# Kernel optimization log

Hardware: AMD Instinct MI355X
Metric: run time of the kernel (lower is better)

The kernel has to match this reference:

```python
import math
import jax, jax.numpy as jnp
import numpy as np

B, S, HID, H, NREL = 4, 512, 1024, 16, 64
D = HID // H  # per-head size = 64, must equal relation embedding dim


def setup_inputs() -> dict:
    key = jax.random.key(0)
    ks = jax.random.split(key, 12)
    w = lambda k, shape: jax.random.normal(k, shape, jnp.float32) * 0.02
    return {
        "q_in": jax.random.normal(ks[0], (B, S, HID), jnp.float32),
        "k_in": jax.random.normal(ks[1], (B, S, HID), jnp.float32),
        "v_in": jax.random.normal(ks[2], (B, S, HID), jnp.float32),
        "mask": jax.random.randint(ks[3], (B, 1, S, S), 0, NREL),
        "Wq": w(ks[4], (HID, HID)), "bq": jnp.zeros((HID,), jnp.float32),
        "Wk": w(ks[5], (HID, HID)), "bk": jnp.zeros((HID,), jnp.float32),
        "Wv": w(ks[6], (HID, HID)), "bv": jnp.zeros((HID,), jnp.float32),
        "Wo": w(ks[7], (HID, HID)), "bo": jnp.zeros((HID,), jnp.float32),
        "rel_k_table": w(ks[8], (NREL, D)),
        "rel_v_table": w(ks[9], (NREL, D)),
    }


def reference(q_in, k_in, v_in, mask, Wq, bq, Wk, bk, Wv, bv, Wo, bo,
              rel_k_table, rel_v_table):
    def proj(x, W, b):  # [B,S,HID] -> [B,H,S,D]
        return (x @ W.T + b).reshape(B, S, H, D).transpose(0, 2, 1, 3)

    q = proj(q_in, Wq, bq)
    k = proj(k_in, Wk, bk)
    v = proj(v_in, Wv, bv)

    ids = mask[:, 0]                      # [B,S,S] relation ids
    rel_k = rel_k_table[ids]              # [B,S,S,D]
    rel_v = rel_v_table[ids]              # [B,S,S,D]

    scores = jnp.einsum('bhqd,bhkd->bhqk', q, k)
    scores = scores + jnp.einsum('bhqd,bqkd->bhqk', q, rel_k) / 4.0
    scores = scores / math.sqrt(float(D))

    bias = (1.0 - (mask > 0).astype(scores.dtype)) * -10000.0  # [B,1,S,S]
    probs = jax.nn.softmax(scores + bias, axis=-1)             # [B,H,S,S]

    out = jnp.einsum('bhqk,bhkd->bhqd', probs, v)
    out = out + 0.25 * jnp.einsum('bhqk,bqkd->bhqd', probs, rel_v)
    out = out.transpose(0, 2, 1, 3).reshape(B, S, HID)
    return out @ Wo.T + bo
```

## Files before the change

kernel.cpp:

```cpp
#include <hip/hip_runtime.h>


typedef __attribute__((ext_vector_type(8))) short bf16x8 __attribute__((may_alias));
typedef __attribute__((ext_vector_type(4))) float f32x4;

__device__ __forceinline__ short f2bf(float x) {
    unsigned u = __float_as_uint(x);
    u += 0x7fff + ((u >> 16) & 1);
    return (short)(u >> 16);
}

__device__ __forceinline__ void async16(void* lds, const void* g) {
    __builtin_amdgcn_global_load_lds(
        (const __attribute__((address_space(1))) void*)g,
        (__attribute__((address_space(3))) void*)lds, 16, 0, 0);
}

__global__ __launch_bounds__(256)
void cast_all(const float* __restrict__ x0, const float* __restrict__ x1, const float* __restrict__ x2,
              const float* __restrict__ w0, const float* __restrict__ w1,
              const float* __restrict__ w2, const float* __restrict__ w3,
              const float* __restrict__ rk, const float* __restrict__ rv,
              const int* __restrict__ mask,
              short* __restrict__ y0, short* __restrict__ y1, short* __restrict__ y2,
              short* __restrict__ u0, short* __restrict__ u1,
              short* __restrict__ u2, short* __restrict__ u3,
              short* __restrict__ rkb, short* __restrict__ rvT,
              unsigned char* __restrict__ mu8)
{
    size_t i = (size_t)blockIdx.x * 256 + threadIdx.x;
    if (i < 2621440u) {
        const float* src; short* dst; size_t off;
        if (i < 3u*524288u) {
            int s = (int)(i / 524288u); off = i % 524288u;
            src = s == 0 ? x0 : (s == 1 ? x1 : x2);
            dst = s == 0 ? y0 : (s == 1 ? y1 : y2);
        } else {
            size_t j = i - 3u*524288u;
            int s = (int)(j / 262144u); off = j % 262144u;
            src = s == 0 ? w0 : (s == 1 ? w1 : (s == 2 ? w2 : w3));
            dst = s == 0 ? u0 : (s == 1 ? u1 : (s == 2 ? u2 : u3));
        }
        float4 f = ((const float4*)src)[off];
        short4 o; o.x = f2bf(f.x); o.y = f2bf(f.y); o.z = f2bf(f.z); o.w = f2bf(f.w);
        ((short4*)dst)[off] = o;
    } else if (i < 2621440u + 1024u) {
        size_t off = i - 2621440u;
        float4 f = ((const float4*)rk)[off];
        short4 o; o.x = f2bf(f.x); o.y = f2bf(f.y); o.z = f2bf(f.z); o.w = f2bf(f.w);
        ((short4*)rkb)[off] = o;
    } else if (i < 2622464u + 1024u) {
        int m = (int)(i - 2622464u);
        int d = m >> 4, r0 = (m & 15) * 4;
        short4 o;
        o.x = f2bf(rv[(size_t)(r0 + 0) * 64 + d]);
        o.y = f2bf(rv[(size_t)(r0 + 1) * 64 + d]);
        o.z = f2bf(rv[(size_t)(r0 + 2) * 64 + d]);
        o.w = f2bf(rv[(size_t)(r0 + 3) * 64 + d]);
        *(short4*)&rvT[d * 64 + r0] = o;
    } else if (i < 2623488u + 262144u) {
        size_t m = i - 2623488u;
        int4 v = ((const int4*)mask)[m];
        uchar4 o;
        o.x = (unsigned char)v.x; o.y = (unsigned char)v.y;
        o.z = (unsigned char)v.z; o.w = (unsigned char)v.w;
        ((uchar4*)mu8)[m] = o;
    }
}

__global__ __launch_bounds__(256)
void gemm12864(const short* __restrict__ A0, const short* __restrict__ A1, const short* __restrict__ A2,
               const short* __restrict__ B0, const short* __restrict__ B1, const short* __restrict__ B2,
               const float* __restrict__ c0, const float* __restrict__ c1, const float* __restrict__ c2,
               void* __restrict__ O0, void* __restrict__ O1, void* __restrict__ O2,
               int mode)
{
    __shared__ short ldsw[2 * 12288];

    const int z = blockIdx.z;
    const short* A    = z == 0 ? A0 : (z == 1 ? A1 : A2);
    const short* Bm   = z == 0 ? B0 : (z == 1 ? B1 : B2);
    const float* bias = z == 0 ? c0 : (z == 1 ? c1 : c2);
    void*        O    = z == 0 ? O0 : (z == 1 ? O1 : O2);

    const int t = threadIdx.x;
    const int lane = t & 63, w = t >> 6;
    const int wr = w >> 1, wc = w & 1;
    const int quad = lane >> 4, cl = lane & 15;
    const int rowBase = blockIdx.y * 128;
    const int colBase = blockIdx.x * 64;
    const int gl = ((lane & 7) - (lane >> 3)) & 7;

    f32x4 acc[4][2];
#pragma unroll
    for (int i = 0; i < 4; ++i)
#pragma unroll
        for (int j = 0; j < 2; ++j) acc[i][j] = (f32x4){0.f, 0.f, 0.f, 0.f};

    const int rstage = w * 8 + (lane >> 3);
    const short* Ag = A  + (size_t)(rowBase + rstage) * 1024 + gl * 8;
    const short* Bg = Bm + (size_t)(colBase + rstage) * 1024 + gl * 8;

    {
        short* Als = ldsw;
        short* Bls = ldsw + 8192;
#pragma unroll
        for (int i = 0; i < 4; ++i)
            async16(&Als[(i * 32 + w * 8) * 64], Ag + (size_t)i * 32 * 1024);
#pragma unroll
        for (int i = 0; i < 2; ++i)
            async16(&Bls[(i * 32 + w * 8) * 64], Bg + (size_t)i * 32 * 1024);
    }

    for (int it = 0; it < 16; ++it) {
        const int cur = it & 1;
        __syncthreads();
        if (it < 15) {
            short* Als = ldsw + (cur ^ 1) * 12288;
            short* Bls = Als + 8192;
            const int k0 = (it + 1) * 64;
#pragma unroll
            for (int i = 0; i < 4; ++i)
                async16(&Als[(i * 32 + w * 8) * 64], Ag + (size_t)i * 32 * 1024 + k0);
#pragma unroll
            for (int i = 0; i < 2; ++i)
                async16(&Bls[(i * 32 + w * 8) * 64], Bg + (size_t)i * 32 * 1024 + k0);
        }
        const short* Als = ldsw + cur * 12288;
        const short* Bls = Als + 8192;
#pragma unroll
        for (int kk = 0; kk < 2; ++kk) {
            bf16x8 a[4], b[2];
#pragma unroll
            for (int mi = 0; mi < 4; ++mi) {
                int r = wr * 64 + mi * 16 + cl;
                int s = (kk * 4 + quad + r) & 7;
                a[mi] = *(const bf16x8*)&Als[r * 64 + s * 8];
            }
#pragma unroll
            for (int ni = 0; ni < 2; ++ni) {
                int r = wc * 32 + ni * 16 + cl;
                int s = (kk * 4 + quad + r) & 7;
                b[ni] = *(const bf16x8*)&Bls[r * 64 + s * 8];
            }
#pragma unroll
            for (int mi = 0; mi < 4; ++mi)
#pragma unroll
                for (int ni = 0; ni < 2; ++ni)
                    acc[mi][ni] = __builtin_amdgcn_mfma_f32_16x16x32_bf16(
                        a[mi], b[ni], acc[mi][ni], 0, 0, 0);
        }
    }

    if (mode == 0) {
#pragma unroll
        for (int mi = 0; mi < 4; ++mi)
#pragma unroll
            for (int ni = 0; ni < 2; ++ni) {
                int col = colBase + wc * 32 + ni * 16 + cl;
                float bv = bias[col];
#pragma unroll
                for (int reg = 0; reg < 4; ++reg) {
                    int row = rowBase + wr * 64 + mi * 16 + quad * 4 + reg;
                    ((float*)O)[(size_t)row * 1024 + col] = acc[mi][ni][reg] + bv;
                }
            }
        return;
    }

    __syncthreads();
    short* Tls = ldsw;
    if (z == 2) {
#pragma unroll
        for (int mi = 0; mi < 4; ++mi)
#pragma unroll
            for (int ni = 0; ni < 2; ++ni) {
                int d = wc * 32 + ni * 16 + cl;
                float bv = bias[colBase + d];
                short4 pk;
                pk.x = f2bf(acc[mi][ni][0] + bv);
                pk.y = f2bf(acc[mi][ni][1] + bv);
                pk.z = f2bf(acc[mi][ni][2] + bv);
                pk.w = f2bf(acc[mi][ni][3] + bv);
                int sl = wr * 64 + mi * 16 + quad * 4;
                *(short4*)&Tls[d * 136 + sl] = pk;
            }
        __syncthreads();
        int d = t >> 2, s0 = (t & 3) * 32;
        int bb = rowBase >> 9, sBase = rowBase & 511, hh = colBase >> 6;
        short* dst = (short*)O + (((size_t)(bb * 16 + hh) * 64 + d) << 9) + sBase + s0;
#pragma unroll
        for (int j = 0; j < 4; ++j)
            *(bf16x8*)(dst + j * 8) = *(const bf16x8*)&Tls[d * 136 + s0 + j * 8];
    } else {
#pragma unroll
        for (int mi = 0; mi < 4; ++mi)
#pragma unroll
            for (int ni = 0; ni < 2; ++ni) {
                int d = wc * 32 + ni * 16 + cl;
                float bv = bias[colBase + d];
#pragma unroll
                for (int reg = 0; reg < 4; ++reg) {
                    int sl = wr * 64 + mi * 16 + quad * 4 + reg;
                    Tls[sl * 72 + d] = f2bf(acc[mi][ni][reg] + bv);
                }
            }
        __syncthreads();
        int sl = t >> 1, half = t & 1;
        int bb = rowBase >> 9, sBase = rowBase & 511, hh = colBase >> 6;
        short* dst = (short*)O + (((size_t)(bb * 16 + hh) * 512 + sBase + sl) << 6) + half * 32;
#pragma unroll
        for (int j = 0; j < 4; ++j)
            *(bf16x8*)(dst + j * 8) = *(const bf16x8*)&Tls[sl * 72 + half * 32 + j * 8];
    }
}

#define AT_BINS 4352
#define AT_PST  8704
#define AT_SLICE 11264

__global__ __launch_bounds__(256)
void attn_kernel(const short* __restrict__ qg, const short* __restrict__ kg,
                 const short* __restrict__ vtg, const unsigned char* __restrict__ mu8,
                 const short* __restrict__ relkb, const short* __restrict__ relvT,
                 short* __restrict__ attn_b)
{
    __shared__ __align__(16) char pool[4 * AT_SLICE];
    const int t = threadIdx.x;
    const int lane = t & 63, w = t >> 6;
    char* mypool = pool + w * AT_SLICE;
    float* qwr    = (float*)mypool;
    float* bins   = (float*)(mypool + AT_BINS);
    short* Pst    = (short*)(mypool + AT_PST);
    short* binsBf = Pst;

    const int quad = lane >> 4, cl = lane & 15;
    const int bid = blockIdx.x;
    const int bh = bid & 63, qq = bid >> 6;
    const int b = bh >> 4, h = bh & 15, q0 = qq * 64 + w * 16;

    const short* qbase = qg  + ((size_t)bh * 512 + q0) * 64;
    const short* kbase = kg  + (size_t)bh * 512 * 64;
    const short* vbase = vtg + (size_t)bh * 64 * 512;
    const unsigned char* mb = mu8 + (size_t)b * 512 * 512 + (size_t)q0 * 512;

    for (int i = lane; i < 16 * 68; i += 64) bins[i] = 0.f;

    bf16x8 qa0 = *(const bf16x8*)(qbase + cl * 64 + quad * 8);
    bf16x8 qa1 = *(const bf16x8*)(qbase + cl * 64 + 32 + quad * 8);

#pragma unroll
    for (int rt = 0; rt < 4; ++rt) {
        const short* kp = relkb + (size_t)(rt * 16 + cl) * 64 + quad * 8;
        bf16x8 rb0 = *(const bf16x8*)kp;
        bf16x8 rb1 = *(const bf16x8*)(kp + 32);
        f32x4 qr = (f32x4){0.f, 0.f, 0.f, 0.f};
        qr = __builtin_amdgcn_mfma_f32_16x16x32_bf16(qa0, rb0, qr, 0, 0, 0);
        qr = __builtin_amdgcn_mfma_f32_16x16x32_bf16(qa1, rb1, qr, 0, 0, 0);
#pragma unroll
        for (int reg = 0; reg < 4; ++reg)
            qwr[(quad * 4 + reg) * 68 + rt * 16 + cl] = qr[reg];
    }

    f32x4 oacc[4];
#pragma unroll
    for (int dt = 0; dt < 4; ++dt) oacc[dt] = (f32x4){0.f, 0.f, 0.f, 0.f};
    float lpart[4] = {0.f, 0.f, 0.f, 0.f};

    for (int c = 0; c < 8; ++c) {
        const int k0 = c * 64;
        int ids[4][4];
#pragma unroll
        for (int nt = 0; nt < 4; ++nt)
#pragma unroll
            for (int reg = 0; reg < 4; ++reg)
                ids[nt][reg] = mb[(size_t)(quad * 4 + reg) * 512 + k0 + nt * 16 + cl];

        bf16x8 vb[8];
#pragma unroll
        for (int dt = 0; dt < 4; ++dt) {
            const short* vp = vbase + (size_t)(dt * 16 + cl) * 512 + k0 + quad * 8;
            vb[dt * 2]     = *(const bf16x8*)vp;
            vb[dt * 2 + 1] = *(const bf16x8*)(vp + 32);
        }

#pragma unroll
        for (int nt = 0; nt < 4; ++nt) {
            const int kidx = k0 + nt * 16 + cl;
            const short* kp = kbase + (size_t)kidx * 64 + quad * 8;
            bf16x8 kb0 = *(const bf16x8*)kp;
            bf16x8 kb1 = *(const bf16x8*)(kp + 32);
            f32x4 s = (f32x4){0.f, 0.f, 0.f, 0.f};
            __builtin_amdgcn_s_setprio(1);
            s = __builtin_amdgcn_mfma_f32_16x16x32_bf16(qa0, kb0, s, 0, 0, 0);
            s = __builtin_amdgcn_mfma_f32_16x16x32_bf16(qa1, kb1, s, 0, 0, 0);
            __builtin_amdgcn_s_setprio(0);
#pragma unroll
            for (int reg = 0; reg < 4; ++reg) {
                int q = quad * 4 + reg;
                int id = ids[nt][reg];
                float sc = (s[reg] + 0.25f * qwr[q * 68 + id]) * 0.125f;
                float p = (id == 0) ? 0.f : __expf(sc);
                lpart[reg] += p;
                atomicAdd(&bins[q * 68 + id], p);
                Pst[q * 72 + nt * 16 + cl] = f2bf(p);
            }
        }
        bf16x8 pa0 = *(const bf16x8*)&Pst[cl * 72 + quad * 8];
        bf16x8 pa1 = *(const bf16x8*)&Pst[cl * 72 + 32 + quad * 8];
        __builtin_amdgcn_s_setprio(1);
#pragma unroll
        for (int dt = 0; dt < 4; ++dt) {
            oacc[dt] = __builtin_amdgcn_mfma_f32_16x16x32_bf16(pa0, vb[dt * 2],     oacc[dt], 0, 0, 0);
            oacc[dt] = __builtin_amdgcn_mfma_f32_16x16x32_bf16(pa1, vb[dt * 2 + 1], oacc[dt], 0, 0, 0);
        }
        __builtin_amdgcn_s_setprio(0);
    }

    float invq[4];
#pragma unroll
    for (int reg = 0; reg < 4; ++reg) {
        float l = lpart[reg];
#pragma unroll
        for (int m = 8; m >= 1; m >>= 1) l += __shfl_xor(l, m);
        invq[reg] = 1.0f / l;
    }

    {
        int q = lane >> 2, r0 = (lane & 3) * 16;
#pragma unroll
        for (int j = 0; j < 4; ++j) {
            float4 f = *(const float4*)&bins[q * 68 + r0 + j * 4];
            short4 o;
            o.x = f2bf(f.x); o.y = f2bf(f.y); o.z = f2bf(f.z); o.w = f2bf(f.w);
            *(short4*)&binsBf[q * 72 + r0 + j * 4] = o;
        }
    }

    bf16x8 ba0 = *(const bf16x8*)&binsBf[cl * 72 + quad * 8];
    bf16x8 ba1 = *(const bf16x8*)&binsBf[cl * 72 + 32 + quad * 8];
#pragma unroll
    for (int dt = 0; dt < 4; ++dt) {
        const short* rp = relvT + (size_t)(dt * 16 + cl) * 64 + quad * 8;
        bf16x8 rv0 = *(const bf16x8*)rp;
        bf16x8 rv1 = *(const bf16x8*)(rp + 32);
        f32x4 racc = (f32x4){0.f, 0.f, 0.f, 0.f};
        racc = __builtin_amdgcn_mfma_f32_16x16x32_bf16(ba0, rv0, racc, 0, 0, 0);
        racc = __builtin_amdgcn_mfma_f32_16x16x32_bf16(ba1, rv1, racc, 0, 0, 0);
#pragma unroll
        for (int reg = 0; reg < 4; ++reg) {
            int q = quad * 4 + reg;
            float val = (oacc[dt][reg] + 0.25f * racc[reg]) * invq[reg];
            attn_b[(size_t)(b * 512 + q0 + q) * 1024 + h * 64 + dt * 16 + cl] = f2bf(val);
        }
    }
}

extern "C" void kernel_launch(void* const* d_in, const int* in_sizes, int n_in,
                              void* d_out, int out_size, void* d_ws, size_t ws_size,
                              hipStream_t stream)
{
    const float* q_in = (const float*)d_in[0];
    const float* k_in = (const float*)d_in[1];
    const float* v_in = (const float*)d_in[2];
    const int*   mask = (const int*)d_in[3];
    const float* Wq   = (const float*)d_in[4];
    const float* bq   = (const float*)d_in[5];
    const float* Wk   = (const float*)d_in[6];
    const float* bk   = (const float*)d_in[7];
    const float* Wv   = (const float*)d_in[8];
    const float* bv   = (const float*)d_in[9];
    const float* Wo   = (const float*)d_in[10];
    const float* bo   = (const float*)d_in[11];
    const float* relk = (const float*)d_in[12];
    const float* relv = (const float*)d_in[13];

    char* ws = (char*)d_ws;
    short* qb     = (short*)(ws);
    short* kb     = (short*)(ws + (4u  << 20));
    short* vt     = (short*)(ws + (8u  << 20));
    short* attn_b = (short*)(ws + (12u << 20));
    short* Xq     = (short*)(ws + (16u << 20));
    short* Xk     = (short*)(ws + (20u << 20));
    short* Xv     = (short*)(ws + (24u << 20));
    short* Wqb    = (short*)(ws + (28u << 20));
    short* Wkb    = (short*)(ws + (30u << 20));
    short* Wvb    = (short*)(ws + (32u << 20));
    short* Wob    = (short*)(ws + (34u << 20));
    short* relkb  = (short*)(ws + (36u << 20));
    short* relvT  = (short*)(ws + (36u << 20) + 8192);
    unsigned char* masku8 = (unsigned char*)(ws + (36u << 20) + 16384);

    cast_all<<<11272, 256, 0, stream>>>(q_in, k_in, v_in, Wq, Wk, Wv, Wo, relk, relv, mask,
                                        Xq, Xk, Xv, Wqb, Wkb, Wvb, Wob, relkb, relvT, masku8);

    gemm12864<<<dim3(16, 16, 3), 256, 0, stream>>>(
        Xq, Xk, Xv, Wqb, Wkb, Wvb, bq, bk, bv, qb, kb, vt, 1);

    attn_kernel<<<dim3(512), 256, 0, stream>>>(qb, kb, vt, masku8, relkb, relvT, attn_b);

    gemm12864<<<dim3(16, 16, 1), 256, 0, stream>>>(
        attn_b, attn_b, attn_b, Wob, Wob, Wob, bo, bo, bo,
        (void*)d_out, (void*)d_out, (void*)d_out, 0);
}
```

Baseline: 236.4 us.

## Stage K and V tiles in LDS with double-buffered async loads

The attention kernel now loads each 64-key K chunk and V^T chunk into shared LDS buffers with async global-to-LDS copies, split across the four waves. It uses XOR-swizzled layouts and double buffering, so the next chunk is prefetched while the current one is computed. This removes the redundant per-wave global reads of K and V, which were previously repeated four times per block. In exchange it adds a block-wide barrier per chunk and more LDS per block, which may lower occupancy.

```diff
diff --git a/kernel.cpp b/kernel.cpp
--- a/kernel.cpp
+++ b/kernel.cpp
@@ -215,9 +215,9 @@
     }
 }
 
-#define AT_BINS 4352
-#define AT_PST  8704
-#define AT_SLICE 11264
+#define AT_KV    16384
+#define AT_WSLC  11264
+#define AT_TOT   (2 * AT_KV + 4 * AT_WSLC)
 
 __global__ __launch_bounds__(256)
 void attn_kernel(const short* __restrict__ qg, const short* __restrict__ kg,
@@ -225,16 +225,16 @@
                  const short* __restrict__ relkb, const short* __restrict__ relvT,
                  short* __restrict__ attn_b)
 {
-    __shared__ __align__(16) char pool[4 * AT_SLICE];
+    __shared__ __align__(16) char pool[AT_TOT];
     const int t = threadIdx.x;
     const int lane = t & 63, w = t >> 6;
-    char* mypool = pool + w * AT_SLICE;
+    const int quad = lane >> 4, cl = lane & 15;
+    char* mypool = pool + 2 * AT_KV + w * AT_WSLC;
     float* qwr    = (float*)mypool;
-    float* bins   = (float*)(mypool + AT_BINS);
-    short* Pst    = (short*)(mypool + AT_PST);
+    float* bins   = (float*)(mypool + 4352);
+    short* Pst    = (short*)(mypool + 8704);
     short* binsBf = Pst;
 
-    const int quad = lane >> 4, cl = lane & 15;
     const int bid = blockIdx.x;
     const int bh = bid & 63, qq = bid >> 6;
     const int b = bh >> 4, h = bh & 15, q0 = qq * 64 + w * 16;
@@ -244,7 +244,18 @@
     const short* vbase = vtg + (size_t)bh * 64 * 512;
     const unsigned char* mb = mu8 + (size_t)b * 512 * 512 + (size_t)q0 * 512;
 
+    const int rA = w * 16 + (lane >> 3);
+    const int rB = rA + 8;
+    const int mmS = lane & 7;
+    const int cA = (mmS ^ (rA & 7)) << 3;
+    const int cB = (mmS ^ (rB & 7)) << 3;
+
     for (int i = lane; i < 16 * 68; i += 64) bins[i] = 0.f;
+
+    async16(pool + w * 2048,               kbase + (size_t)rA * 64 + cA);
+    async16(pool + w * 2048 + 1024,        kbase + (size_t)rB * 64 + cB);
+    async16(pool + 8192 + w * 2048,        vbase + (size_t)rA * 512 + cA);
+    async16(pool + 8192 + w * 2048 + 1024, vbase + (size_t)rB * 512 + cB);
 
     bf16x8 qa0 = *(const bf16x8*)(qbase + cl * 64 + quad * 8);
     bf16x8 qa1 = *(const bf16x8*)(qbase + cl * 64 + 32 + quad * 8);
@@ -268,7 +279,19 @@
     float lpart[4] = {0.f, 0.f, 0.f, 0.f};
 
     for (int c = 0; c < 8; ++c) {
+        const int cur = c & 1;
         const int k0 = c * 64;
+        __syncthreads();
+
+        if (c < 7) {
+            const int k1 = k0 + 64;
+            char* nb = pool + (cur ^ 1) * AT_KV;
+            async16(nb + w * 2048,               kbase + (size_t)(k1 + rA) * 64 + cA);
+            async16(nb + w * 2048 + 1024,        kbase + (size_t)(k1 + rB) * 64 + cB);
+            async16(nb + 8192 + w * 2048,        vbase + (size_t)rA * 512 + k1 + cA);
+            async16(nb + 8192 + w * 2048 + 1024, vbase + (size_t)rB * 512 + k1 + cB);
+        }
+
         int ids[4][4];
 #pragma unroll
         for (int nt = 0; nt < 4; ++nt)
@@ -276,20 +299,14 @@
             for (int reg = 0; reg < 4; ++reg)
                 ids[nt][reg] = mb[(size_t)(quad * 4 + reg) * 512 + k0 + nt * 16 + cl];
 
-        bf16x8 vb[8];
-#pragma unroll
-        for (int dt = 0; dt < 4; ++dt) {
-            const short* vp = vbase + (size_t)(dt * 16 + cl) * 512 + k0 + quad * 8;
-            vb[dt * 2]     = *(const bf16x8*)vp;
-            vb[dt * 2 + 1] = *(const bf16x8*)(vp + 32);
-        }
+        const char* Kt = pool + cur * AT_KV;
+        const char* Vt = Kt + 8192;
 
 #pragma unroll
         for (int nt = 0; nt < 4; ++nt) {
-            const int kidx = k0 + nt * 16 + cl;
-            const short* kp = kbase + (size_t)kidx * 64 + quad * 8;
-            bf16x8 kb0 = *(const bf16x8*)kp;
-            bf16x8 kb1 = *(const bf16x8*)(kp + 32);
+            const int rk = nt * 16 + cl;
+            bf16x8 kb0 = *(const bf16x8*)(Kt + rk * 128 + ((quad ^ (rk & 7)) << 4));
+            bf16x8 kb1 = *(const bf16x8*)(Kt + rk * 128 + (((quad + 4) ^ (rk & 7)) << 4));
             f32x4 s = (f32x4){0.f, 0.f, 0.f, 0.f};
             __builtin_amdgcn_s_setprio(1);
             s = __builtin_amdgcn_mfma_f32_16x16x32_bf16(qa0, kb0, s, 0, 0, 0);
@@ -311,8 +328,11 @@
         __builtin_amdgcn_s_setprio(1);
 #pragma unroll
         for (int dt = 0; dt < 4; ++dt) {
-            oacc[dt] = __builtin_amdgcn_mfma_f32_16x16x32_bf16(pa0, vb[dt * 2],     oacc[dt], 0, 0, 0);
-            oacc[dt] = __builtin_amdgcn_mfma_f32_16x16x32_bf16(pa1, vb[dt * 2 + 1], oacc[dt], 0, 0, 0);
+            const int rv = dt * 16 + cl;
+            bf16x8 vb0 = *(const bf16x8*)(Vt + rv * 128 + ((quad ^ (rv & 7)) << 4));
+            bf16x8 vb1 = *(const bf16x8*)(Vt + rv * 128 + (((quad + 4) ^ (rv & 7)) << 4));
+            oacc[dt] = __builtin_amdgcn_mfma_f32_16x16x32_bf16(pa0, vb0, oacc[dt], 0, 0, 0);
+            oacc[dt] = __builtin_amdgcn_mfma_f32_16x16x32_bf16(pa1, vb1, oacc[dt], 0, 0, 0);
         }
         __builtin_amdgcn_s_setprio(0);
     }
```

Measured after the change: 237.2 us. Within noise of the previous version (+0.3%).

## Split attention key range across two waves per query tile and grid-stride cast kernel

Applied to the files above, without the earlier changes.

The attention kernel now gives each block a single 16-query tile handled by two waves, each covering half of the 512 keys. A shared-memory reduction then combines the partial outputs, row sums and relation bins before the rel_v MFMA and the store. The grid grows from 512 to 2048 blocks of 128 threads, which gives more parallelism and shorter per-wave loops on the GPU's many CUs. The cost is two block barriers and duplicated q·rel_k work per wave. The cast kernel also switches to a grid-stride loop over 2048 blocks.

```diff
diff --git a/kernel.cpp b/kernel.cpp
--- a/kernel.cpp
+++ b/kernel.cpp
@@ -16,6 +16,7 @@
         (__attribute__((address_space(3))) void*)lds, 16, 0, 0);
 }
 
+#define CAST_TOTAL 2885632u
 __global__ __launch_bounds__(256)
 void cast_all(const float* __restrict__ x0, const float* __restrict__ x1, const float* __restrict__ x2,
               const float* __restrict__ w0, const float* __restrict__ w1,
@@ -28,43 +29,45 @@
               short* __restrict__ rkb, short* __restrict__ rvT,
               unsigned char* __restrict__ mu8)
 {
-    size_t i = (size_t)blockIdx.x * 256 + threadIdx.x;
-    if (i < 2621440u) {
-        const float* src; short* dst; size_t off;
-        if (i < 3u*524288u) {
-            int s = (int)(i / 524288u); off = i % 524288u;
-            src = s == 0 ? x0 : (s == 1 ? x1 : x2);
-            dst = s == 0 ? y0 : (s == 1 ? y1 : y2);
+    const size_t stride = (size_t)gridDim.x * 256;
+    for (size_t i = (size_t)blockIdx.x * 256 + threadIdx.x; i < CAST_TOTAL; i += stride) {
+        if (i < 2621440u) {
+            const float* src; short* dst; size_t off;
+            if (i < 3u*524288u) {
+                int s = (int)(i / 524288u); off = i % 524288u;
+                src = s == 0 ? x0 : (s == 1 ? x1 : x2);
+                dst = s == 0 ? y0 : (s == 1 ? y1 : y2);
+            } else {
+                size_t j = i - 3u*524288u;
+                int s = (int)(j / 262144u); off = j % 262144u;
+                src = s == 0 ? w0 : (s == 1 ? w1 : (s == 2 ? w2 : w3));
+                dst = s == 0 ? u0 : (s == 1 ? u1 : (s == 2 ? u2 : u3));
+            }
+            float4 f = ((const float4*)src)[off];
+            short4 o; o.x = f2bf(f.x); o.y = f2bf(f.y); o.z = f2bf(f.z); o.w = f2bf(f.w);
+            ((short4*)dst)[off] = o;
+        } else if (i < 2621440u + 1024u) {
+            size_t off = i - 2621440u;
+            float4 f = ((const float4*)rk)[off];
+            short4 o; o.x = f2bf(f.x); o.y = f2bf(f.y); o.z = f2bf(f.z); o.w = f2bf(f.w);
+            ((short4*)rkb)[off] = o;
+        } else if (i < 2622464u + 1024u) {
+            int m = (int)(i - 2622464u);
+            int d = m >> 4, r0 = (m & 15) * 4;
+            short4 o;
+            o.x = f2bf(rv[(size_t)(r0 + 0) * 64 + d]);
+            o.y = f2bf(rv[(size_t)(r0 + 1) * 64 + d]);
+            o.z = f2bf(rv[(size_t)(r0 + 2) * 64 + d]);
+            o.w = f2bf(rv[(size_t)(r0 + 3) * 64 + d]);
+            *(short4*)&rvT[d * 64 + r0] = o;
         } else {
-            size_t j = i - 3u*524288u;
-            int s = (int)(j / 262144u); off = j % 262144u;
-            src = s == 0 ? w0 : (s == 1 ? w1 : (s == 2 ? w2 : w3));
-            dst = s == 0 ? u0 : (s == 1 ? u1 : (s == 2 ? u2 : u3));
-        }
-        float4 f = ((const float4*)src)[off];
-        short4 o; o.x = f2bf(f.x); o.y = f2bf(f.y); o.z = f2bf(f.z); o.w = f2bf(f.w);
-        ((short4*)dst)[off] = o;
-    } else if (i < 2621440u + 1024u) {
-        size_t off = i - 2621440u;
-        float4 f = ((const float4*)rk)[off];
-        short4 o; o.x = f2bf(f.x); o.y = f2bf(f.y); o.z = f2bf(f.z); o.w = f2bf(f.w);
-        ((short4*)rkb)[off] = o;
-    } else if (i < 2622464u + 1024u) {
-        int m = (int)(i - 2622464u);
-        int d = m >> 4, r0 = (m & 15) * 4;
-        short4 o;
-        o.x = f2bf(rv[(size_t)(r0 + 0) * 64 + d]);
-        o.y = f2bf(rv[(size_t)(r0 + 1) * 64 + d]);
-        o.z = f2bf(rv[(size_t)(r0 + 2) * 64 + d]);
-        o.w = f2bf(rv[(size_t)(r0 + 3) * 64 + d]);
-        *(short4*)&rvT[d * 64 + r0] = o;
-    } else if (i < 2623488u + 262144u) {
-        size_t m = i - 2623488u;
-        int4 v = ((const int4*)mask)[m];
-        uchar4 o;
-        o.x = (unsigned char)v.x; o.y = (unsigned char)v.y;
-        o.z = (unsigned char)v.z; o.w = (unsigned char)v.w;
-        ((uchar4*)mu8)[m] = o;
+            size_t m = i - 2623488u;
+            int4 v = ((const int4*)mask)[m];
+            uchar4 o;
+            o.x = (unsigned char)v.x; o.y = (unsigned char)v.y;
+            o.z = (unsigned char)v.z; o.w = (unsigned char)v.w;
+            ((uchar4*)mu8)[m] = o;
+        }
     }
 }
 
@@ -215,29 +218,32 @@
     }
 }
 
-#define AT_BINS 4352
-#define AT_PST  8704
-#define AT_SLICE 11264
-
-__global__ __launch_bounds__(256)
+#define AT_QWR   0
+#define AT_BINS  4352
+#define AT_PST   13056
+#define AT_TOT   17664
+
+__global__ __launch_bounds__(128, 4)
 void attn_kernel(const short* __restrict__ qg, const short* __restrict__ kg,
                  const short* __restrict__ vtg, const unsigned char* __restrict__ mu8,
                  const short* __restrict__ relkb, const short* __restrict__ relvT,
                  short* __restrict__ attn_b)
 {
-    __shared__ __align__(16) char pool[4 * AT_SLICE];
+    __shared__ __align__(16) char pool[AT_TOT];
     const int t = threadIdx.x;
     const int lane = t & 63, w = t >> 6;
-    char* mypool = pool + w * AT_SLICE;
-    float* qwr    = (float*)mypool;
-    float* bins   = (float*)(mypool + AT_BINS);
-    short* Pst    = (short*)(mypool + AT_PST);
-    short* binsBf = Pst;
-
     const int quad = lane >> 4, cl = lane & 15;
+
+    float* qwr    = (float*)(pool + AT_QWR);
+    float* bins   = (float*)(pool + AT_BINS + w * 4352);
+    short* Pst    = (short*)(pool + AT_PST  + w * 2304);
+    float* qwrF   = (float*)(pool + AT_QWR);
+    float* lsum1  = (float*)(pool + AT_PST + 2304);
+    short* binsBf = (short*)(pool + AT_PST);
+
     const int bid = blockIdx.x;
-    const int bh = bid & 63, qq = bid >> 6;
-    const int b = bh >> 4, h = bh & 15, q0 = qq * 64 + w * 16;
+    const int bh = bid & 63, qt = bid >> 6;
+    const int b = bh >> 4, h = bh & 15, q0 = qt * 16;
 
     const short* qbase = qg  + ((size_t)bh * 512 + q0) * 64;
     const short* kbase = kg  + (size_t)bh * 512 * 64;
@@ -267,8 +273,8 @@
     for (int dt = 0; dt < 4; ++dt) oacc[dt] = (f32x4){0.f, 0.f, 0.f, 0.f};
     float lpart[4] = {0.f, 0.f, 0.f, 0.f};
 
-    for (int c = 0; c < 8; ++c) {
-        const int k0 = c * 64;
+    for (int c = 0; c < 4; ++c) {
+        const int k0 = w * 256 + c * 64;
         int ids[4][4];
 #pragma unroll
         for (int nt = 0; nt < 4; ++nt)
@@ -317,41 +323,74 @@
         __builtin_amdgcn_s_setprio(0);
     }
 
-    float invq[4];
+    float lred[4];
 #pragma unroll
     for (int reg = 0; reg < 4; ++reg) {
         float l = lpart[reg];
 #pragma unroll
         for (int m = 8; m >= 1; m >>= 1) l += __shfl_xor(l, m);
-        invq[reg] = 1.0f / l;
-    }
-
-    {
-        int q = lane >> 2, r0 = (lane & 3) * 16;
-#pragma unroll
-        for (int j = 0; j < 4; ++j) {
-            float4 f = *(const float4*)&bins[q * 68 + r0 + j * 4];
-            short4 o;
-            o.x = f2bf(f.x); o.y = f2bf(f.y); o.z = f2bf(f.z); o.w = f2bf(f.w);
-            *(short4*)&binsBf[q * 72 + r0 + j * 4] = o;
-        }
-    }
-
-    bf16x8 ba0 = *(const bf16x8*)&binsBf[cl * 72 + quad * 8];
-    bf16x8 ba1 = *(const bf16x8*)&binsBf[cl * 72 + 32 + quad * 8];
-#pragma unroll
-    for (int dt = 0; dt < 4; ++dt) {
-        const short* rp = relvT + (size_t)(dt * 16 + cl) * 64 + quad * 8;
-        bf16x8 rv0 = *(const bf16x8*)rp;
-        bf16x8 rv1 = *(const bf16x8*)(rp + 32);
-        f32x4 racc = (f32x4){0.f, 0.f, 0.f, 0.f};
-        racc = __builtin_amdgcn_mfma_f32_16x16x32_bf16(ba0, rv0, racc, 0, 0, 0);
-        racc = __builtin_amdgcn_mfma_f32_16x16x32_bf16(ba1, rv1, racc, 0, 0, 0);
-#pragma unroll
-        for (int reg = 0; reg < 4; ++reg) {
-            int q = quad * 4 + reg;
-            float val = (oacc[dt][reg] + 0.25f * racc[reg]) * invq[reg];
-            attn_b[(size_t)(b * 512 + q0 + q) * 1024 + h * 64 + dt * 16 + cl] = f2bf(val);
+        lred[reg] = l;
+    }
+
+    __syncthreads();
+
+    if (w == 1) {
+        if (cl == 0) {
+#pragma unroll
+            for (int reg = 0; reg < 4; ++reg)
+                lsum1[quad * 4 + reg] = lred[reg];
+        }
+#pragma unroll
+        for (int dt = 0; dt < 4; ++dt)
+#pragma unroll
+            for (int reg = 0; reg < 4; ++reg)
+                qwrF[(quad * 4 + reg) * 68 + dt * 16 + cl] = oacc[dt][reg];
+    }
+
+    __syncthreads();
+
+    if (w == 0) {
+        float invq[4];
+#pragma unroll
+        for (int reg = 0; reg < 4; ++reg)
+            invq[reg] = 1.0f / (lred[reg] + lsum1[quad * 4 + reg]);
+#pragma unroll
+        for (int dt = 0; dt < 4; ++dt)
+#pragma unroll
+            for (int reg = 0; reg < 4; ++reg)
+                oacc[dt][reg] += qwrF[(quad * 4 + reg) * 68 + dt * 16 + cl];
+
+        {
+            int q = lane >> 2, r0 = (lane & 3) * 16;
+            const float* bins0 = (const float*)(pool + AT_BINS);
+            const float* bins1 = (const float*)(pool + AT_BINS + 4352);
+#pragma unroll
+            for (int j = 0; j < 4; ++j) {
+                float4 fa = *(const float4*)&bins0[q * 68 + r0 + j * 4];
+                float4 fb = *(const float4*)&bins1[q * 68 + r0 + j * 4];
+                short4 o;
+                o.x = f2bf(fa.x + fb.x); o.y = f2bf(fa.y + fb.y);
+                o.z = f2bf(fa.z + fb.z); o.w = f2bf(fa.w + fb.w);
+                *(short4*)&binsBf[q * 72 + r0 + j * 4] = o;
+            }
+        }
+
+        bf16x8 ba0 = *(const bf16x8*)&binsBf[cl * 72 + quad * 8];
+        bf16x8 ba1 = *(const bf16x8*)&binsBf[cl * 72 + 32 + quad * 8];
+#pragma unroll
+        for (int dt = 0; dt < 4; ++dt) {
+            const short* rp = relvT + (size_t)(dt * 16 + cl) * 64 + quad * 8;
+            bf16x8 rv0 = *(const bf16x8*)rp;
+            bf16x8 rv1 = *(const bf16x8*)(rp + 32);
+            f32x4 racc = (f32x4){0.f, 0.f, 0.f, 0.f};
+            racc = __builtin_amdgcn_mfma_f32_16x16x32_bf16(ba0, rv0, racc, 0, 0, 0);
+            racc = __builtin_amdgcn_mfma_f32_16x16x32_bf16(ba1, rv1, racc, 0, 0, 0);
+#pragma unroll
+            for (int reg = 0; reg < 4; ++reg) {
+                int q = quad * 4 + reg;
+                float val = (oacc[dt][reg] + 0.25f * racc[reg]) * invq[reg];
+                attn_b[(size_t)(b * 512 + q0 + q) * 1024 + h * 64 + dt * 16 + cl] = f2bf(val);
+            }
         }
     }
 }
@@ -391,13 +430,13 @@
     short* relvT  = (short*)(ws + (36u << 20) + 8192);
     unsigned char* masku8 = (unsigned char*)(ws + (36u << 20) + 16384);
 
-    cast_all<<<11272, 256, 0, stream>>>(q_in, k_in, v_in, Wq, Wk, Wv, Wo, relk, relv, mask,
-                                        Xq, Xk, Xv, Wqb, Wkb, Wvb, Wob, relkb, relvT, masku8);
+    cast_all<<<2048, 256, 0, stream>>>(q_in, k_in, v_in, Wq, Wk, Wv, Wo, relk, relv, mask,
+                                       Xq, Xk, Xv, Wqb, Wkb, Wvb, Wob, relkb, relvT, masku8);
 
     gemm12864<<<dim3(16, 16, 3), 256, 0, stream>>>(
         Xq, Xk, Xv, Wqb, Wkb, Wvb, bq, bk, bv, qb, kb, vt, 1);
 
-    attn_kernel<<<dim3(512), 256, 0, stream>>>(qb, kb, vt, masku8, relkb, relvT, attn_b);
+    attn_kernel<<<dim3(2048), 128, 0, stream>>>(qb, kb, vt, masku8, relkb, relvT, attn_b);
 
     gemm12864<<<dim3(16, 16, 1), 256, 0, stream>>>(
         attn_b, attn_b, attn_b, Wob, Wob, Wob, bo, bo, bo,
```

Result: slower. 248.2 us (+5.0%).
